# Kernel tuning notes

Measured on AMD Instinct MI355X. Metric: run time of the kernel, lower is better.

Reference implementation:

```python
import jax, jax.numpy as jnp
import numpy as np

HIDDEN = 1024
FFN = 3584
N_EXPERTS = 8
TOP_K = 2


def setup_inputs() -> dict:
    key = jax.random.key(0)
    ks = jax.random.split(key, 5)
    B, S = 2, 2048
    hidden_states = jax.random.normal(ks[0], (B, S, HIDDEN), dtype=jnp.float32)
    # gate: Linear(hidden, n_experts, bias=False); stored as [H, E] so y = x @ gate_w
    gate_w = jax.random.normal(ks[1], (HIDDEN, N_EXPERTS), dtype=jnp.float32) * (HIDDEN ** -0.5)
    # stacked expert weights: w1 (gate proj), w3 (up proj): [E, H, F]; w2 (down proj): [E, F, H]
    w1 = jax.random.normal(ks[2], (N_EXPERTS, HIDDEN, FFN), dtype=jnp.float32) * (HIDDEN ** -0.5)
    w3 = jax.random.normal(ks[3], (N_EXPERTS, HIDDEN, FFN), dtype=jnp.float32) * (HIDDEN ** -0.5)
    w2 = jax.random.normal(ks[4], (N_EXPERTS, FFN, HIDDEN), dtype=jnp.float32) * (FFN ** -0.5)
    return {"hidden_states": hidden_states, "gate_w": gate_w, "w1": w1, "w2": w2, "w3": w3}


def reference(hidden_states, gate_w, w1, w2, w3):
    B, S, H = hidden_states.shape
    x = hidden_states.reshape(-1, H)  # [T, H]
    T = x.shape[0]
    router_logits = x @ gate_w  # [T, E]
    # softmax in fp32 as in original
    routing_weights = jax.nn.softmax(router_logits.astype(jnp.float32), axis=-1)
    top_w, selected = jax.lax.top_k(routing_weights, TOP_K)  # [T, k]
    top_w = top_w / jnp.sum(top_w, axis=-1, keepdims=True)
    top_w = top_w.astype(x.dtype)
    # scatter top-k weights into dense per-expert combine weights [T, E];
    # zero weight for unselected experts reproduces the sparse gather/scatter math exactly
    combine = jnp.zeros((T, N_EXPERTS), dtype=x.dtype).at[
        jnp.arange(T)[:, None], selected
    ].add(top_w)
    # expert gated MLP, all experts batched: [T, E, F]
    g = jnp.einsum('th,ehf->tef', x, w1)
    u = jnp.einsum('th,ehf->tef', x, w3)
    h = jax.nn.silu(g) * u
    # down-proj fused with weighted combine: avoids [T, E, H] intermediate
    final_hidden_states = jnp.einsum('tef,efh,te->th', h, w2, combine)
    return final_hidden_states, router_logits
```

## Files before the change

kernel.cpp:

```cpp
#include <hip/hip_runtime.h>
#include <hip/hip_bf16.h>
#include <cstdint>
#include <cstddef>

#define T_TOK 4096
#define HID   1024
#define FFN   3584
#define FFI   (2 * FFN)
#define NEXP  8
#define RTOT  (T_TOK * 2)
#define MAXT  72
#define BM 128
#define BN 128
#define BK 64
#define NT1 (FFI / BN)
#define NT2 (HID / BN)
#define SPLITK2 2
#define KCH2 (FFN / SPLITK2)
#define CPAD 32

typedef __attribute__((ext_vector_type(8))) short bvec8;
typedef __attribute__((ext_vector_type(4))) short bvec4;
typedef __attribute__((ext_vector_type(4))) float fvec4;
typedef unsigned short u16;

__device__ __forceinline__ u16 f2b(float f) {
  __bf16 b = (__bf16)f;
  return __builtin_bit_cast(u16, b);
}
__device__ __forceinline__ float b2f(u16 u) {
  unsigned v = (unsigned)u << 16;
  return __builtin_bit_cast(float, v);
}

__device__ __forceinline__ void gload16(const u16* g, u16* l) {
  __builtin_amdgcn_global_load_lds((const __attribute__((address_space(1))) void*)g,
                                   (__attribute__((address_space(3))) void*)l, 16, 0, 0);
}

__device__ __forceinline__ int xcd_swz(int bid, int nwg) {
  int q = nwg >> 3, r = nwg & 7;
  int xcd = bid & 7, sub = bid >> 3;
  return (xcd < r ? xcd * (q + 1) : r * (q + 1) + (xcd - r) * q) + sub;
}

__global__ void router_kernel(const float* __restrict__ x, const float* __restrict__ gw,
                              float* __restrict__ logits, int* __restrict__ tk_id,
                              float* __restrict__ tk_w, int* __restrict__ counts,
                              u16* __restrict__ xb, int full) {
  const int lane = threadIdx.x & 63;
  const int wid  = threadIdx.x >> 6;
  const int t = blockIdx.x * 4 + wid;
  const float4* xr = (const float4*)(x + (size_t)t * HID);
  float acc[NEXP] = {0.f, 0.f, 0.f, 0.f, 0.f, 0.f, 0.f, 0.f};
#pragma unroll
  for (int it = 0; it < 4; ++it) {
    int k4 = it * 64 + lane;
    float4 xv = xr[k4];
    if (xb) {
      bvec4 o;
      o[0] = (short)f2b(xv.x); o[1] = (short)f2b(xv.y);
      o[2] = (short)f2b(xv.z); o[3] = (short)f2b(xv.w);
      *(bvec4*)(xb + (size_t)t * HID + k4 * 4) = o;
    }
    const float* gp = gw + (size_t)k4 * 4 * NEXP;
    float xs[4] = {xv.x, xv.y, xv.z, xv.w};
#pragma unroll
    for (int kk = 0; kk < 4; ++kk) {
      float4 ga = ((const float4*)(gp + kk * NEXP))[0];
      float4 gb = ((const float4*)(gp + kk * NEXP))[1];
      acc[0] += xs[kk] * ga.x; acc[1] += xs[kk] * ga.y;
      acc[2] += xs[kk] * ga.z; acc[3] += xs[kk] * ga.w;
      acc[4] += xs[kk] * gb.x; acc[5] += xs[kk] * gb.y;
      acc[6] += xs[kk] * gb.z; acc[7] += xs[kk] * gb.w;
    }
  }
#pragma unroll
  for (int off = 32; off > 0; off >>= 1) {
#pragma unroll
    for (int e = 0; e < NEXP; ++e) acc[e] += __shfl_xor(acc[e], off, 64);
  }
  if (lane < NEXP) logits[(size_t)t * NEXP + lane] = acc[lane];
  if (full && lane == 0) {
    int e0 = 0; float l0 = acc[0];
#pragma unroll
    for (int e = 1; e < NEXP; ++e) if (acc[e] > l0) { l0 = acc[e]; e0 = e; }
    int e1 = -1; float l1 = -3.4e38f;
#pragma unroll
    for (int e = 0; e < NEXP; ++e) if (e != e0 && acc[e] > l1) { l1 = acc[e]; e1 = e; }
    float w0 = 1.f / (1.f + expf(l1 - l0));
    float w1 = 1.f - w0;
    tk_id[t * 2 + 0] = e0; tk_id[t * 2 + 1] = e1;
    tk_w[t * 2 + 0] = w0;  tk_w[t * 2 + 1] = w1;
    atomicAdd(&counts[e0 * CPAD], 1); atomicAdd(&counts[e1 * CPAD], 1);
  }
}

__global__ void scan_kernel(const int* __restrict__ counts, int* __restrict__ offsets,
                            int* __restrict__ cursors, int4* __restrict__ tilemap) {
  __shared__ int c[NEXP];
  __shared__ int tbase[NEXP + 1];
  const int t = threadIdx.x;
  if (t < NEXP) c[t] = counts[t * CPAD];
  __syncthreads();
  if (t < NEXP) {
    int off = 0, tiles = 0;
    for (int e = 0; e < t; ++e) { off += c[e]; tiles += (c[e] + BM - 1) / BM; }
    offsets[t] = off; cursors[t * CPAD] = 0;
    if (t == NEXP - 1) {
      offsets[NEXP] = off + c[t];
      tbase[NEXP] = tiles + (c[t] + BM - 1) / BM;
    }
    tbase[t] = tiles;
    const int cc = c[t];
    for (int tm = 0; tm * BM < cc; ++tm)
      tilemap[tiles + tm] = make_int4(t, off + tm * BM, min(BM, cc - tm * BM), 0);
  }
  __syncthreads();
  for (int i = tbase[NEXP] + t; i < MAXT; i += 64)
    tilemap[i] = make_int4(-1, 0, 0, 0);
}

__global__ void scatter_kernel(const int* __restrict__ tk_id, const float* __restrict__ tk_w,
                               const int* __restrict__ offsets, int* __restrict__ cursors,
                               int* __restrict__ rowmap, float* __restrict__ roww,
                               int* __restrict__ tokrow) {
  int i = blockIdx.x * 256 + threadIdx.x;
  int t = i >> 1;
  int e = tk_id[i]; float w = tk_w[i];
  const int lane = threadIdx.x & 63;
  const unsigned long long lt = (lane == 63) ? ~0ull >> 1 : (1ull << lane) - 1ull;
  int base = 0, rank = 0;
#pragma unroll
  for (int ex = 0; ex < NEXP; ++ex) {
    unsigned long long m = __ballot(e == ex);
    if (e == ex) {
      int cnt = __popcll(m);
      int leader = __ffsll((long long)m) - 1;
      int b = 0;
      if (lane == leader) b = atomicAdd(&cursors[ex * CPAD], cnt);
      b = __shfl(b, leader, 64);
      base = b; rank = __popcll(m & lt);
    }
  }
  int r = offsets[e] + base + rank;
  rowmap[r] = t; roww[r] = w;
  tokrow[i] = r;
}

__global__ void transpose_cast_dual_kernel(const float* __restrict__ w1,
                                           const float* __restrict__ w3,
                                           u16* __restrict__ bi) {
  __shared__ __attribute__((aligned(16))) u16 tile[64 * 72];
  const int z = blockIdx.z, e = z >> 1, half = z & 1;
  const float* src = (half ? w3 : w1) + (size_t)e * HID * FFN;
  u16* dst = bi + (size_t)e * FFI * HID;
  const int c0 = blockIdx.x * 64, r0 = blockIdx.y * 64;
  const int t = threadIdx.x;
  const int m = t & 15;
  const int g = t >> 4;
  u16 v[4][4];
#pragma unroll
  for (int i = 0; i < 4; ++i) {
    float4 q = *(const float4*)(src + (size_t)(r0 + 4 * g + i) * FFN + c0 + 4 * m);
    v[i][0] = f2b(q.x); v[i][1] = f2b(q.y); v[i][2] = f2b(q.z); v[i][3] = f2b(q.w);
  }
  const int phys = (g ^ ((m & 3) << 2)) * 4;
#pragma unroll
  for (int j = 0; j < 4; ++j) {
    int c = 4 * m + j;
    bvec4 o; o[0] = (short)v[0][j]; o[1] = (short)v[1][j];
    o[2] = (short)v[2][j]; o[3] = (short)v[3][j];
    *(bvec4*)&tile[c * 72 + phys] = o;
  }
  __syncthreads();
  const int cl = t >> 2;
  const int q  = t & 3;
  const int base = ((q ^ ((cl >> 2) & 3)) << 4);
  bvec8 ra = *(const bvec8*)&tile[cl * 72 + base];
  bvec8 rb = *(const bvec8*)&tile[cl * 72 + base + 8];
  const int orow = (c0 << 1) + ((cl >> 4) << 5) + (cl & 15) + (half << 4);
  u16* dp = dst + (size_t)orow * HID + r0 + 16 * q;
  *(bvec8*)(dp + 0) = ra;
  *(bvec8*)(dp + 8) = rb;
}

__global__ void transpose_cast_w2_kernel(const float* __restrict__ w2, u16* __restrict__ w2t) {
  __shared__ __attribute__((aligned(16))) u16 tile[64 * 72];
  const int e = blockIdx.z;
  const float* src = w2 + (size_t)e * FFN * HID;
  u16* dst = w2t + (size_t)e * HID * FFN;
  const int c0 = blockIdx.x * 64, r0 = blockIdx.y * 64;
  const int t = threadIdx.x;
  const int m = t & 15;
  const int g = t >> 4;
  u16 v[4][4];
#pragma unroll
  for (int i = 0; i < 4; ++i) {
    float4 q = *(const float4*)(src + (size_t)(r0 + 4 * g + i) * HID + c0 + 4 * m);
    v[i][0] = f2b(q.x); v[i][1] = f2b(q.y); v[i][2] = f2b(q.z); v[i][3] = f2b(q.w);
  }
  const int phys = (g ^ ((m & 3) << 2)) * 4;
#pragma unroll
  for (int j = 0; j < 4; ++j) {
    int c = 4 * m + j;
    bvec4 o; o[0] = (short)v[0][j]; o[1] = (short)v[1][j];
    o[2] = (short)v[2][j]; o[3] = (short)v[3][j];
    *(bvec4*)&tile[c * 72 + phys] = o;
  }
  __syncthreads();
  const int cl = t >> 2;
  const int q  = t & 3;
  const int base = ((q ^ ((cl >> 2) & 3)) << 4);
  bvec8 ra = *(const bvec8*)&tile[cl * 72 + base];
  bvec8 rb = *(const bvec8*)&tile[cl * 72 + base + 8];
  u16* dp = dst + (size_t)(c0 + cl) * FFN + r0 + 16 * q;
  *(bvec8*)(dp + 0) = ra;
  *(bvec8*)(dp + 8) = rb;
}

__launch_bounds__(256, 3)
__global__ void gemm1_kernel(const u16* __restrict__ xb, const u16* __restrict__ bi,
                             const int* __restrict__ rowmap,
                             const int4* __restrict__ tilemap, u16* __restrict__ hbuf) {
  const int wg = xcd_swz(blockIdx.x, NT1 * MAXT);
  const int mt = wg % MAXT;
  const int nt = wg / MAXT;
  int4 ti = tilemap[mt];
  if (ti.x < 0) return;
  const int e = ti.x, rowbase = ti.y, mvalid = ti.z;
  const int n0 = nt * BN;

  __shared__ __attribute__((aligned(128))) u16 As[BM * BK];
  __shared__ __attribute__((aligned(128))) u16 Bs[BN * BK];

  const int tid = threadIdx.x;
  const int lane = tid & 63;
  const int wv = tid >> 6;

  const int srow = tid >> 3;
  const int csrc = ((tid & 7) ^ (srow & 7)) * 8;
  const u16* wb = bi + (size_t)e * FFI * HID;
  const u16* gA[4]; const u16* gB[4];
  u16* lA[4]; u16* lB[4];
#pragma unroll
  for (int r = 0; r < 4; ++r) {
    int row = r * 32 + srow;
    int tok = rowmap[min(rowbase + row, RTOT - 1)];
    gA[r] = xb + (size_t)tok * HID + csrc;
    gB[r] = wb + (size_t)(n0 + row) * HID + csrc;
    lA[r] = &As[(r * 32 + wv * 8) * BK];
    lB[r] = &Bs[(r * 32 + wv * 8) * BK];
  }

  const int wm = (tid >> 7) & 1, wn = (tid >> 6) & 1;
  const int l15 = lane & 15;
  const int kg = lane >> 4;
  const int swz = l15 & 7;
  const int aBase = (wm * 64 + l15) * BK;
  const int bBase = (wn * 64 + l15) * BK;
  const int ch0 = ((0 + kg) ^ swz) * 8;
  const int ch1 = ((4 + kg) ^ swz) * 8;

  fvec4 acc[4][4] = {};

  for (int kt = 0; kt < HID / BK; ++kt) {
#pragma unroll
    for (int r = 0; r < 4; ++r) { gload16(gA[r], lA[r]); gA[r] += BK; }
#pragma unroll
    for (int r = 0; r < 4; ++r) { gload16(gB[r], lB[r]); gB[r] += BK; }
    __syncthreads();
    bvec8 a0[4], a1[4];
#pragma unroll
    for (int mi = 0; mi < 4; ++mi) {
      a0[mi] = *(const bvec8*)&As[aBase + mi * 16 * BK + ch0];
      a1[mi] = *(const bvec8*)&As[aBase + mi * 16 * BK + ch1];
    }
#pragma unroll
    for (int ni = 0; ni < 4; ++ni) {
      bvec8 b0 = *(const bvec8*)&Bs[bBase + ni * 16 * BK + ch0];
#pragma unroll
      for (int mi = 0; mi < 4; ++mi)
        acc[mi][ni] = __builtin_amdgcn_mfma_f32_16x16x32_bf16(a0[mi], b0, acc[mi][ni], 0, 0, 0);
      bvec8 b1 = *(const bvec8*)&Bs[bBase + ni * 16 * BK + ch1];
#pragma unroll
      for (int mi = 0; mi < 4; ++mi)
        acc[mi][ni] = __builtin_amdgcn_mfma_f32_16x16x32_bf16(a1[mi], b1, acc[mi][ni], 0, 0, 0);
    }
    __syncthreads();
  }
  const int rg4 = (lane >> 4) * 4;
#pragma unroll
  for (int mi = 0; mi < 4; ++mi) {
#pragma unroll
    for (int j = 0; j < 4; ++j) {
      int ml = wm * 64 + mi * 16 + rg4 + j;
      if (ml < mvalid) {
        size_t rowoff = (size_t)(rowbase + ml) * FFN + ((n0 + wn * 64) >> 1);
#pragma unroll
        for (int np = 0; np < 2; ++np) {
          float g = acc[mi][2 * np][j], u = acc[mi][2 * np + 1][j];
          float hv = (g / (1.f + expf(-g))) * u;
          hbuf[rowoff + np * 16 + l15] = f2b(hv);
        }
      }
    }
  }
}

__launch_bounds__(256, 3)
__global__ void gemm2_kernel(const u16* __restrict__ hbuf, const u16* __restrict__ w2t,
                             const float* __restrict__ roww,
                             const int4* __restrict__ tilemap, u16* __restrict__ part) {
  const int wg = xcd_swz(blockIdx.x, NT2 * MAXT * SPLITK2);
  const int mt = wg % MAXT;
  const int rest = wg / MAXT;
  const int nt = rest % NT2;
  const int sk = rest / NT2;
  int4 ti = tilemap[mt];
  if (ti.x < 0) return;
  const int e = ti.x, rowbase = ti.y, mvalid = ti.z;
  const int n0 = nt * BN;
  const int k0 = sk * KCH2;

  __shared__ __attribute__((aligned(128))) u16 As[BM * BK];
  __shared__ __attribute__((aligned(128))) u16 Bs[BN * BK];

  const int tid = threadIdx.x;
  const int lane = tid & 63;
  const int wv = tid >> 6;

  const int srow = tid >> 3;
  const int csrc = ((tid & 7) ^ (srow & 7)) * 8;
  const u16* wb2 = w2t + (size_t)e * HID * FFN;
  const u16* gA[4]; const u16* gB[4];
  u16* lA[4]; u16* lB[4];
#pragma unroll
  for (int r = 0; r < 4; ++r) {
    int row = r * 32 + srow;
    gA[r] = hbuf + (size_t)min(rowbase + row, RTOT - 1) * FFN + k0 + csrc;
    gB[r] = wb2 + (size_t)(n0 + row) * FFN + k0 + csrc;
    lA[r] = &As[(r * 32 + wv * 8) * BK];
    lB[r] = &Bs[(r * 32 + wv * 8) * BK];
  }

  const int wm = (tid >> 7) & 1, wn = (tid >> 6) & 1;
  const int l15 = lane & 15;
  const int kg = lane >> 4;
  const int swz = l15 & 7;
  const int aBase = (wm * 64 + l15) * BK;
  const int bBase = (wn * 64 + l15) * BK;
  const int ch0 = ((0 + kg) ^ swz) * 8;
  const int ch1 = ((4 + kg) ^ swz) * 8;

  fvec4 acc[4][4] = {};

  for (int kt = 0; kt < KCH2 / BK; ++kt) {
#pragma unroll
    for (int r = 0; r < 4; ++r) { gload16(gA[r], lA[r]); gA[r] += BK; }
#pragma unroll
    for (int r = 0; r < 4; ++r) { gload16(gB[r], lB[r]); gB[r] += BK; }
    __syncthreads();
    bvec8 a0[4], a1[4];
#pragma unroll
    for (int mi = 0; mi < 4; ++mi) {
      a0[mi] = *(const bvec8*)&As[aBase + mi * 16 * BK + ch0];
      a1[mi] = *(const bvec8*)&As[aBase + mi * 16 * BK + ch1];
    }
#pragma unroll
    for (int ni = 0; ni < 4; ++ni) {
      bvec8 b0 = *(const bvec8*)&Bs[bBase + ni * 16 * BK + ch0];
#pragma unroll
      for (int mi = 0; mi < 4; ++mi)
        acc[mi][ni] = __builtin_amdgcn_mfma_f32_16x16x32_bf16(a0[mi], b0, acc[mi][ni], 0, 0, 0);
      bvec8 b1 = *(const bvec8*)&Bs[bBase + ni * 16 * BK + ch1];
#pragma unroll
      for (int mi = 0; mi < 4; ++mi)
        acc[mi][ni] = __builtin_amdgcn_mfma_f32_16x16x32_bf16(a1[mi], b1, acc[mi][ni], 0, 0, 0);
    }
    __syncthreads();
  }
  u16* pp = part + (size_t)sk * RTOT * HID;
  const int rg4 = (lane >> 4) * 4;
#pragma unroll
  for (int mi = 0; mi < 4; ++mi) {
#pragma unroll
    for (int j = 0; j < 4; ++j) {
      int ml = wm * 64 + mi * 16 + rg4 + j;
      if (ml < mvalid) {
        int r = rowbase + ml;
        float wgt = roww[r];
        u16* op = pp + (size_t)r * HID + n0 + wn * 64;
#pragma unroll
        for (int ni = 0; ni < 4; ++ni)
          op[ni * 16 + l15] = f2b(acc[mi][ni][j] * wgt);
      }
    }
  }
}

__global__ void combine_kernel(const u16* __restrict__ part, const int* __restrict__ tokrow,
                               float* __restrict__ out) {
  int idx = blockIdx.x * 256 + threadIdx.x;
  int t = idx >> 7;
  int c = (idx & 127) * 8;
  int r0 = tokrow[2 * t], r1 = tokrow[2 * t + 1];
  const size_t sk1 = (size_t)RTOT * HID;
  bvec8 a = *(const bvec8*)(part + (size_t)r0 * HID + c);
  bvec8 b = *(const bvec8*)(part + sk1 + (size_t)r0 * HID + c);
  bvec8 d = *(const bvec8*)(part + (size_t)r1 * HID + c);
  bvec8 f = *(const bvec8*)(part + sk1 + (size_t)r1 * HID + c);
  float* dst = out + (size_t)t * HID + c;
#pragma unroll
  for (int k = 0; k < 8; ++k)
    dst[k] = (b2f((u16)a[k]) + b2f((u16)b[k])) + (b2f((u16)d[k]) + b2f((u16)f[k]));
}

extern "C" void kernel_launch(void* const* d_in, const int* in_sizes, int n_in,
                              void* d_out, int out_size, void* d_ws, size_t ws_size,
                              hipStream_t stream) {
  (void)in_sizes; (void)n_in; (void)out_size;
  const float* x  = (const float*)d_in[0];
  const float* gw = (const float*)d_in[1];
  const float* w1 = (const float*)d_in[2];
  const float* w2 = (const float*)d_in[3];
  const float* w3 = (const float*)d_in[4];
  float* out = (float*)d_out;
  float* logits = out + (size_t)T_TOK * HID;

  size_t off = 0;
  auto take = [&](size_t b) { size_t o = off; off += (b + 255) & ~(size_t)255; return o; };
  size_t o_xb   = take((size_t)T_TOK * HID * 2);
  size_t o_wt   = take((size_t)NEXP * FFI * HID * 2);
  size_t o_hb   = take((size_t)RTOT * FFN * 2);
  size_t o_rmap = take((size_t)RTOT * 4);
  size_t o_rw   = take((size_t)RTOT * 4);
  size_t o_tid  = take((size_t)RTOT * 4);
  size_t o_tw   = take((size_t)RTOT * 4);
  size_t o_trow = take((size_t)RTOT * 4);
  size_t o_cnt  = take(4 * NEXP * CPAD);
  size_t o_ofs  = take(4 * (NEXP + 1));
  size_t o_cur  = take(4 * NEXP * CPAD);
  size_t o_tmap = take(MAXT * 16);
  size_t total = off;

  if (ws_size < total) {
    hipMemsetAsync(d_out, 0, (size_t)T_TOK * HID * sizeof(float), stream);
    router_kernel<<<T_TOK / 4, 256, 0, stream>>>(x, gw, logits, nullptr, nullptr, nullptr,
                                                 nullptr, 0);
    return;
  }

  char* w = (char*)d_ws;
  u16* xb   = (u16*)(w + o_xb);
  u16* bi   = (u16*)(w + o_wt);
  u16* w2t  = bi;
  u16* part = bi + (size_t)NEXP * HID * FFN;
  u16* hb   = (u16*)(w + o_hb);
  int*   rmap = (int*)(w + o_rmap);
  float* rw   = (float*)(w + o_rw);
  int*   tkid = (int*)(w + o_tid);
  float* tkw  = (float*)(w + o_tw);
  int*   trow = (int*)(w + o_trow);
  int*   cnt  = (int*)(w + o_cnt);
  int*   ofs  = (int*)(w + o_ofs);
  int*   cur  = (int*)(w + o_cur);
  int4*  tmap = (int4*)(w + o_tmap);

  hipMemsetAsync(cnt, 0, 4 * NEXP * CPAD, stream);
  router_kernel<<<T_TOK / 4, 256, 0, stream>>>(x, gw, logits, tkid, tkw, cnt, xb, 1);
  scan_kernel<<<1, 64, 0, stream>>>(cnt, ofs, cur, tmap);
  scatter_kernel<<<RTOT / 256, 256, 0, stream>>>(tkid, tkw, ofs, cur, rmap, rw, trow);
  transpose_cast_dual_kernel<<<dim3(FFN / 64, HID / 64, 2 * NEXP), 256, 0, stream>>>(w1, w3, bi);
  gemm1_kernel<<<NT1 * MAXT, 256, 0, stream>>>(xb, bi, rmap, tmap, hb);
  transpose_cast_w2_kernel<<<dim3(HID / 64, FFN / 64, NEXP), 256, 0, stream>>>(w2, w2t);
  gemm2_kernel<<<NT2 * MAXT * SPLITK2, 256, 0, stream>>>(hb, w2t, rw, tmap, part);
  combine_kernel<<<T_TOK * HID / 8 / 256, 256, 0, stream>>>(part, trow, out);
}
```

Measured before the change: 384.8 us.

## Merge router with w1/w3 transpose and gemm1 with w2 transpose into fused launches

Combines the router and the w1/w3 transpose-cast into one grid that branches on block index, and likewise runs the w2 transpose-cast blocks alongside the gemm1 blocks in one launch. To make this legal, w2t gets its own workspace region instead of aliasing the w1/w3 buffer that gemm1 reads. The aim is to remove launch gaps and let memory-bound transpose work overlap with router and GEMM compute. The cost is extra workspace and shared fused kernels with a larger grid. The fused kernel uses the gemm1 launch bounds and shared-memory footprint for the transpose blocks.

```diff
diff --git a/kernel.cpp b/kernel.cpp
--- a/kernel.cpp
+++ b/kernel.cpp
@@ -18,6 +18,10 @@
 #define SPLITK2 2
 #define KCH2 (FFN / SPLITK2)
 #define CPAD 32
+#define G1BLKS (NT1 * MAXT)
+#define W2TBLKS ((HID/64)*(FFN/64)*NEXP)
+#define RTRBLKS (T_TOK / 4)
+#define DTBLKS  ((FFN/64)*(HID/64)*2*NEXP)
 
 typedef __attribute__((ext_vector_type(8))) short bvec8;
 typedef __attribute__((ext_vector_type(4))) short bvec4;
@@ -44,13 +48,14 @@
   return (xcd < r ? xcd * (q + 1) : r * (q + 1) + (xcd - r) * q) + sub;
 }
 
-__global__ void router_kernel(const float* __restrict__ x, const float* __restrict__ gw,
-                              float* __restrict__ logits, int* __restrict__ tk_id,
-                              float* __restrict__ tk_w, int* __restrict__ counts,
-                              u16* __restrict__ xb, int full) {
-  const int lane = threadIdx.x & 63;
-  const int wid  = threadIdx.x >> 6;
-  const int t = blockIdx.x * 4 + wid;
+
+__device__ void router_body(const float* __restrict__ x, const float* __restrict__ gw,
+                            float* __restrict__ logits, int* __restrict__ tk_id,
+                            float* __restrict__ tk_w, int* __restrict__ counts,
+                            u16* __restrict__ xb, int blk, int tid) {
+  const int lane = tid & 63;
+  const int wid  = tid >> 6;
+  const int t = blk * 4 + wid;
   const float4* xr = (const float4*)(x + (size_t)t * HID);
   float acc[NEXP] = {0.f, 0.f, 0.f, 0.f, 0.f, 0.f, 0.f, 0.f};
 #pragma unroll
@@ -81,7 +86,7 @@
     for (int e = 0; e < NEXP; ++e) acc[e] += __shfl_xor(acc[e], off, 64);
   }
   if (lane < NEXP) logits[(size_t)t * NEXP + lane] = acc[lane];
-  if (full && lane == 0) {
+  if (tk_id && lane == 0) {
     int e0 = 0; float l0 = acc[0];
 #pragma unroll
     for (int e = 1; e < NEXP; ++e) if (acc[e] > l0) { l0 = acc[e]; e0 = e; }
@@ -94,6 +99,218 @@
     tk_w[t * 2 + 0] = w0;  tk_w[t * 2 + 1] = w1;
     atomicAdd(&counts[e0 * CPAD], 1); atomicAdd(&counts[e1 * CPAD], 1);
   }
+}
+
+__device__ void dualT_body(const float* __restrict__ w1, const float* __restrict__ w3,
+                           u16* __restrict__ bi, int bx, int by, int bz, int t,
+                           u16* __restrict__ tile) {
+  const int e = bz >> 1, half = bz & 1;
+  const float* src = (half ? w3 : w1) + (size_t)e * HID * FFN;
+  u16* dst = bi + (size_t)e * FFI * HID;
+  const int c0 = bx * 64, r0 = by * 64;
+  const int m = t & 15;
+  const int g = t >> 4;
+  u16 v[4][4];
+#pragma unroll
+  for (int i = 0; i < 4; ++i) {
+    float4 q = *(const float4*)(src + (size_t)(r0 + 4 * g + i) * FFN + c0 + 4 * m);
+    v[i][0] = f2b(q.x); v[i][1] = f2b(q.y); v[i][2] = f2b(q.z); v[i][3] = f2b(q.w);
+  }
+  const int phys = (g ^ ((m & 3) << 2)) * 4;
+#pragma unroll
+  for (int j = 0; j < 4; ++j) {
+    int c = 4 * m + j;
+    bvec4 o; o[0] = (short)v[0][j]; o[1] = (short)v[1][j];
+    o[2] = (short)v[2][j]; o[3] = (short)v[3][j];
+    *(bvec4*)&tile[c * 72 + phys] = o;
+  }
+  __syncthreads();
+  const int cl = t >> 2;
+  const int q  = t & 3;
+  const int base = ((q ^ ((cl >> 2) & 3)) << 4);
+  bvec8 ra = *(const bvec8*)&tile[cl * 72 + base];
+  bvec8 rb = *(const bvec8*)&tile[cl * 72 + base + 8];
+  const int orow = (c0 << 1) + ((cl >> 4) << 5) + (cl & 15) + (half << 4);
+  u16* dp = dst + (size_t)orow * HID + r0 + 16 * q;
+  *(bvec8*)(dp + 0) = ra;
+  *(bvec8*)(dp + 8) = rb;
+}
+
+__device__ void w2T_body(const float* __restrict__ w2, u16* __restrict__ w2t,
+                         int bx, int by, int e, int t, u16* __restrict__ tile) {
+  const float* src = w2 + (size_t)e * FFN * HID;
+  u16* dst = w2t + (size_t)e * HID * FFN;
+  const int c0 = bx * 64, r0 = by * 64;
+  const int m = t & 15;
+  const int g = t >> 4;
+  u16 v[4][4];
+#pragma unroll
+  for (int i = 0; i < 4; ++i) {
+    float4 q = *(const float4*)(src + (size_t)(r0 + 4 * g + i) * HID + c0 + 4 * m);
+    v[i][0] = f2b(q.x); v[i][1] = f2b(q.y); v[i][2] = f2b(q.z); v[i][3] = f2b(q.w);
+  }
+  const int phys = (g ^ ((m & 3) << 2)) * 4;
+#pragma unroll
+  for (int j = 0; j < 4; ++j) {
+    int c = 4 * m + j;
+    bvec4 o; o[0] = (short)v[0][j]; o[1] = (short)v[1][j];
+    o[2] = (short)v[2][j]; o[3] = (short)v[3][j];
+    *(bvec4*)&tile[c * 72 + phys] = o;
+  }
+  __syncthreads();
+  const int cl = t >> 2;
+  const int q  = t & 3;
+  const int base = ((q ^ ((cl >> 2) & 3)) << 4);
+  bvec8 ra = *(const bvec8*)&tile[cl * 72 + base];
+  bvec8 rb = *(const bvec8*)&tile[cl * 72 + base + 8];
+  u16* dp = dst + (size_t)(c0 + cl) * FFN + r0 + 16 * q;
+  *(bvec8*)(dp + 0) = ra;
+  *(bvec8*)(dp + 8) = rb;
+}
+
+__device__ void gemm1_body(const u16* __restrict__ xb, const u16* __restrict__ bi,
+                           const int* __restrict__ rowmap, const int4* __restrict__ tilemap,
+                           u16* __restrict__ hbuf, int bid, int tid,
+                           u16* __restrict__ As, u16* __restrict__ Bs) {
+  const int wg = xcd_swz(bid, NT1 * MAXT);
+  const int mt = wg % MAXT;
+  const int nt = wg / MAXT;
+  int4 ti = tilemap[mt];
+  if (ti.x < 0) return;
+  const int e = ti.x, rowbase = ti.y, mvalid = ti.z;
+  const int n0 = nt * BN;
+
+  const int lane = tid & 63;
+  const int wv = tid >> 6;
+  const int srow = tid >> 3;
+  const int csrc = ((tid & 7) ^ (srow & 7)) * 8;
+  const u16* wb = bi + (size_t)e * FFI * HID;
+  const u16* gA[4]; const u16* gB[4];
+  u16* lA[4]; u16* lB[4];
+#pragma unroll
+  for (int r = 0; r < 4; ++r) {
+    int row = r * 32 + srow;
+    int tok = rowmap[min(rowbase + row, RTOT - 1)];
+    gA[r] = xb + (size_t)tok * HID + csrc;
+    gB[r] = wb + (size_t)(n0 + row) * HID + csrc;
+    lA[r] = &As[(r * 32 + wv * 8) * BK];
+    lB[r] = &Bs[(r * 32 + wv * 8) * BK];
+  }
+
+  const int wm = (tid >> 7) & 1, wn = (tid >> 6) & 1;
+  const int l15 = lane & 15;
+  const int kg = lane >> 4;
+  const int swz = l15 & 7;
+  const int aBase = (wm * 64 + l15) * BK;
+  const int bBase = (wn * 64 + l15) * BK;
+  const int ch0 = ((0 + kg) ^ swz) * 8;
+  const int ch1 = ((4 + kg) ^ swz) * 8;
+
+  fvec4 acc[4][4] = {};
+
+  for (int kt = 0; kt < HID / BK; ++kt) {
+#pragma unroll
+    for (int r = 0; r < 4; ++r) { gload16(gA[r], lA[r]); gA[r] += BK; }
+#pragma unroll
+    for (int r = 0; r < 4; ++r) { gload16(gB[r], lB[r]); gB[r] += BK; }
+    __syncthreads();
+    bvec8 a0[4], a1[4];
+#pragma unroll
+    for (int mi = 0; mi < 4; ++mi) {
+      a0[mi] = *(const bvec8*)&As[aBase + mi * 16 * BK + ch0];
+      a1[mi] = *(const bvec8*)&As[aBase + mi * 16 * BK + ch1];
+    }
+#pragma unroll
+    for (int ni = 0; ni < 4; ++ni) {
+      bvec8 b0 = *(const bvec8*)&Bs[bBase + ni * 16 * BK + ch0];
+#pragma unroll
+      for (int mi = 0; mi < 4; ++mi)
+        acc[mi][ni] = __builtin_amdgcn_mfma_f32_16x16x32_bf16(a0[mi], b0, acc[mi][ni], 0, 0, 0);
+      bvec8 b1 = *(const bvec8*)&Bs[bBase + ni * 16 * BK + ch1];
+#pragma unroll
+      for (int mi = 0; mi < 4; ++mi)
+        acc[mi][ni] = __builtin_amdgcn_mfma_f32_16x16x32_bf16(a1[mi], b1, acc[mi][ni], 0, 0, 0);
+    }
+    __syncthreads();
+  }
+  const int rg4 = (lane >> 4) * 4;
+#pragma unroll
+  for (int mi = 0; mi < 4; ++mi) {
+#pragma unroll
+    for (int j = 0; j < 4; ++j) {
+      int ml = wm * 64 + mi * 16 + rg4 + j;
+      if (ml < mvalid) {
+        size_t rowoff = (size_t)(rowbase + ml) * FFN + ((n0 + wn * 64) >> 1);
+#pragma unroll
+        for (int np = 0; np < 2; ++np) {
+          float g = acc[mi][2 * np][j], u = acc[mi][2 * np + 1][j];
+          float hv = (g / (1.f + expf(-g))) * u;
+          hbuf[rowoff + np * 16 + l15] = f2b(hv);
+        }
+      }
+    }
+  }
+}
+
+
+__global__ void fused_pre_kernel(const float* __restrict__ x, const float* __restrict__ gw,
+                                 const float* __restrict__ w1, const float* __restrict__ w3,
+                                 float* __restrict__ logits, int* __restrict__ tk_id,
+                                 float* __restrict__ tk_w, int* __restrict__ counts,
+                                 u16* __restrict__ xb, u16* __restrict__ bi) {
+  __shared__ __attribute__((aligned(16))) u16 tile[64 * 72];
+  const int bid = blockIdx.x;
+  if (bid < RTRBLKS) {
+    router_body(x, gw, logits, tk_id, tk_w, counts, xb, bid, threadIdx.x);
+  } else {
+    int did = bid - RTRBLKS;
+    int bx = did % (FFN / 64); int rest = did / (FFN / 64);
+    int by = rest % (HID / 64); int bz = rest / (HID / 64);
+    dualT_body(w1, w3, bi, bx, by, bz, threadIdx.x, tile);
+  }
+}
+
+__launch_bounds__(256, 3)
+__global__ void fused_g1w2_kernel(const u16* __restrict__ xb, const u16* __restrict__ bi,
+                                  const int* __restrict__ rowmap,
+                                  const int4* __restrict__ tilemap, u16* __restrict__ hbuf,
+                                  const float* __restrict__ w2, u16* __restrict__ w2t) {
+  __shared__ __attribute__((aligned(128))) u16 As[BM * BK];
+  __shared__ __attribute__((aligned(128))) u16 Bs[BN * BK];
+  const int bid = blockIdx.x;
+  if (bid < G1BLKS) {
+    gemm1_body(xb, bi, rowmap, tilemap, hbuf, bid, threadIdx.x, As, Bs);
+  } else {
+    int id = bid - G1BLKS;
+    int bx = id % (HID / 64); int rest = id / (HID / 64);
+    int by = rest % (FFN / 64); int e = rest / (FFN / 64);
+    w2T_body(w2, w2t, bx, by, e, threadIdx.x, As);
+  }
+}
+
+__global__ void router_kernel(const float* __restrict__ x, const float* __restrict__ gw,
+                              float* __restrict__ logits, int* __restrict__ tk_id,
+                              float* __restrict__ tk_w, int* __restrict__ counts,
+                              u16* __restrict__ xb) {
+  router_body(x, gw, logits, tk_id, tk_w, counts, xb, blockIdx.x, threadIdx.x);
+}
+__global__ void transpose_cast_dual_kernel(const float* __restrict__ w1,
+                                           const float* __restrict__ w3,
+                                           u16* __restrict__ bi) {
+  __shared__ __attribute__((aligned(16))) u16 tile[64 * 72];
+  dualT_body(w1, w3, bi, blockIdx.x, blockIdx.y, blockIdx.z, threadIdx.x, tile);
+}
+__global__ void transpose_cast_w2_kernel(const float* __restrict__ w2, u16* __restrict__ w2t) {
+  __shared__ __attribute__((aligned(16))) u16 tile[64 * 72];
+  w2T_body(w2, w2t, blockIdx.x, blockIdx.y, blockIdx.z, threadIdx.x, tile);
+}
+__launch_bounds__(256, 3)
+__global__ void gemm1_kernel(const u16* __restrict__ xb, const u16* __restrict__ bi,
+                             const int* __restrict__ rowmap,
+                             const int4* __restrict__ tilemap, u16* __restrict__ hbuf) {
+  __shared__ __attribute__((aligned(128))) u16 As[BM * BK];
+  __shared__ __attribute__((aligned(128))) u16 Bs[BN * BK];
+  gemm1_body(xb, bi, rowmap, tilemap, hbuf, blockIdx.x, threadIdx.x, As, Bs);
 }
 
 __global__ void scan_kernel(const int* __restrict__ counts, int* __restrict__ offsets,
@@ -148,166 +365,6 @@
   tokrow[i] = r;
 }
 
-__global__ void transpose_cast_dual_kernel(const float* __restrict__ w1,
-                                           const float* __restrict__ w3,
-                                           u16* __restrict__ bi) {
-  __shared__ __attribute__((aligned(16))) u16 tile[64 * 72];
-  const int z = blockIdx.z, e = z >> 1, half = z & 1;
-  const float* src = (half ? w3 : w1) + (size_t)e * HID * FFN;
-  u16* dst = bi + (size_t)e * FFI * HID;
-  const int c0 = blockIdx.x * 64, r0 = blockIdx.y * 64;
-  const int t = threadIdx.x;
-  const int m = t & 15;
-  const int g = t >> 4;
-  u16 v[4][4];
-#pragma unroll
-  for (int i = 0; i < 4; ++i) {
-    float4 q = *(const float4*)(src + (size_t)(r0 + 4 * g + i) * FFN + c0 + 4 * m);
-    v[i][0] = f2b(q.x); v[i][1] = f2b(q.y); v[i][2] = f2b(q.z); v[i][3] = f2b(q.w);
-  }
-  const int phys = (g ^ ((m & 3) << 2)) * 4;
-#pragma unroll
-  for (int j = 0; j < 4; ++j) {
-    int c = 4 * m + j;
-    bvec4 o; o[0] = (short)v[0][j]; o[1] = (short)v[1][j];
-    o[2] = (short)v[2][j]; o[3] = (short)v[3][j];
-    *(bvec4*)&tile[c * 72 + phys] = o;
-  }
-  __syncthreads();
-  const int cl = t >> 2;
-  const int q  = t & 3;
-  const int base = ((q ^ ((cl >> 2) & 3)) << 4);
-  bvec8 ra = *(const bvec8*)&tile[cl * 72 + base];
-  bvec8 rb = *(const bvec8*)&tile[cl * 72 + base + 8];
-  const int orow = (c0 << 1) + ((cl >> 4) << 5) + (cl & 15) + (half << 4);
-  u16* dp = dst + (size_t)orow * HID + r0 + 16 * q;
-  *(bvec8*)(dp + 0) = ra;
-  *(bvec8*)(dp + 8) = rb;
-}
-
-__global__ void transpose_cast_w2_kernel(const float* __restrict__ w2, u16* __restrict__ w2t) {
-  __shared__ __attribute__((aligned(16))) u16 tile[64 * 72];
-  const int e = blockIdx.z;
-  const float* src = w2 + (size_t)e * FFN * HID;
-  u16* dst = w2t + (size_t)e * HID * FFN;
-  const int c0 = blockIdx.x * 64, r0 = blockIdx.y * 64;
-  const int t = threadIdx.x;
-  const int m = t & 15;
-  const int g = t >> 4;
-  u16 v[4][4];
-#pragma unroll
-  for (int i = 0; i < 4; ++i) {
-    float4 q = *(const float4*)(src + (size_t)(r0 + 4 * g + i) * HID + c0 + 4 * m);
-    v[i][0] = f2b(q.x); v[i][1] = f2b(q.y); v[i][2] = f2b(q.z); v[i][3] = f2b(q.w);
-  }
-  const int phys = (g ^ ((m & 3) << 2)) * 4;
-#pragma unroll
-  for (int j = 0; j < 4; ++j) {
-    int c = 4 * m + j;
-    bvec4 o; o[0] = (short)v[0][j]; o[1] = (short)v[1][j];
-    o[2] = (short)v[2][j]; o[3] = (short)v[3][j];
-    *(bvec4*)&tile[c * 72 + phys] = o;
-  }
-  __syncthreads();
-  const int cl = t >> 2;
-  const int q  = t & 3;
-  const int base = ((q ^ ((cl >> 2) & 3)) << 4);
-  bvec8 ra = *(const bvec8*)&tile[cl * 72 + base];
-  bvec8 rb = *(const bvec8*)&tile[cl * 72 + base + 8];
-  u16* dp = dst + (size_t)(c0 + cl) * FFN + r0 + 16 * q;
-  *(bvec8*)(dp + 0) = ra;
-  *(bvec8*)(dp + 8) = rb;
-}
-
-__launch_bounds__(256, 3)
-__global__ void gemm1_kernel(const u16* __restrict__ xb, const u16* __restrict__ bi,
-                             const int* __restrict__ rowmap,
-                             const int4* __restrict__ tilemap, u16* __restrict__ hbuf) {
-  const int wg = xcd_swz(blockIdx.x, NT1 * MAXT);
-  const int mt = wg % MAXT;
-  const int nt = wg / MAXT;
-  int4 ti = tilemap[mt];
-  if (ti.x < 0) return;
-  const int e = ti.x, rowbase = ti.y, mvalid = ti.z;
-  const int n0 = nt * BN;
-
-  __shared__ __attribute__((aligned(128))) u16 As[BM * BK];
-  __shared__ __attribute__((aligned(128))) u16 Bs[BN * BK];
-
-  const int tid = threadIdx.x;
-  const int lane = tid & 63;
-  const int wv = tid >> 6;
-
-  const int srow = tid >> 3;
-  const int csrc = ((tid & 7) ^ (srow & 7)) * 8;
-  const u16* wb = bi + (size_t)e * FFI * HID;
-  const u16* gA[4]; const u16* gB[4];
-  u16* lA[4]; u16* lB[4];
-#pragma unroll
-  for (int r = 0; r < 4; ++r) {
-    int row = r * 32 + srow;
-    int tok = rowmap[min(rowbase + row, RTOT - 1)];
-    gA[r] = xb + (size_t)tok * HID + csrc;
-    gB[r] = wb + (size_t)(n0 + row) * HID + csrc;
-    lA[r] = &As[(r * 32 + wv * 8) * BK];
-    lB[r] = &Bs[(r * 32 + wv * 8) * BK];
-  }
-
-  const int wm = (tid >> 7) & 1, wn = (tid >> 6) & 1;
-  const int l15 = lane & 15;
-  const int kg = lane >> 4;
-  const int swz = l15 & 7;
-  const int aBase = (wm * 64 + l15) * BK;
-  const int bBase = (wn * 64 + l15) * BK;
-  const int ch0 = ((0 + kg) ^ swz) * 8;
-  const int ch1 = ((4 + kg) ^ swz) * 8;
-
-  fvec4 acc[4][4] = {};
-
-  for (int kt = 0; kt < HID / BK; ++kt) {
-#pragma unroll
-    for (int r = 0; r < 4; ++r) { gload16(gA[r], lA[r]); gA[r] += BK; }
-#pragma unroll
-    for (int r = 0; r < 4; ++r) { gload16(gB[r], lB[r]); gB[r] += BK; }
-    __syncthreads();
-    bvec8 a0[4], a1[4];
-#pragma unroll
-    for (int mi = 0; mi < 4; ++mi) {
-      a0[mi] = *(const bvec8*)&As[aBase + mi * 16 * BK + ch0];
-      a1[mi] = *(const bvec8*)&As[aBase + mi * 16 * BK + ch1];
-    }
-#pragma unroll
-    for (int ni = 0; ni < 4; ++ni) {
-      bvec8 b0 = *(const bvec8*)&Bs[bBase + ni * 16 * BK + ch0];
-#pragma unroll
-      for (int mi = 0; mi < 4; ++mi)
-        acc[mi][ni] = __builtin_amdgcn_mfma_f32_16x16x32_bf16(a0[mi], b0, acc[mi][ni], 0, 0, 0);
-      bvec8 b1 = *(const bvec8*)&Bs[bBase + ni * 16 * BK + ch1];
-#pragma unroll
-      for (int mi = 0; mi < 4; ++mi)
-        acc[mi][ni] = __builtin_amdgcn_mfma_f32_16x16x32_bf16(a1[mi], b1, acc[mi][ni], 0, 0, 0);
-    }
-    __syncthreads();
-  }
-  const int rg4 = (lane >> 4) * 4;
-#pragma unroll
-  for (int mi = 0; mi < 4; ++mi) {
-#pragma unroll
-    for (int j = 0; j < 4; ++j) {
-      int ml = wm * 64 + mi * 16 + rg4 + j;
-      if (ml < mvalid) {
-        size_t rowoff = (size_t)(rowbase + ml) * FFN + ((n0 + wn * 64) >> 1);
-#pragma unroll
-        for (int np = 0; np < 2; ++np) {
-          float g = acc[mi][2 * np][j], u = acc[mi][2 * np + 1][j];
-          float hv = (g / (1.f + expf(-g))) * u;
-          hbuf[rowoff + np * 16 + l15] = f2b(hv);
-        }
-      }
-    }
-  }
-}
-
 __launch_bounds__(256, 3)
 __global__ void gemm2_kernel(const u16* __restrict__ hbuf, const u16* __restrict__ w2t,
                              const float* __restrict__ roww,
@@ -442,19 +499,21 @@
   size_t o_ofs  = take(4 * (NEXP + 1));
   size_t o_cur  = take(4 * NEXP * CPAD);
   size_t o_tmap = take(MAXT * 16);
-  size_t total = off;
-
-  if (ws_size < total) {
+  size_t total_base = off;
+  size_t o_w2t  = take((size_t)NEXP * HID * FFN * 2);
+  size_t total_fused = off;
+
+  if (ws_size < total_base) {
     hipMemsetAsync(d_out, 0, (size_t)T_TOK * HID * sizeof(float), stream);
-    router_kernel<<<T_TOK / 4, 256, 0, stream>>>(x, gw, logits, nullptr, nullptr, nullptr,
-                                                 nullptr, 0);
+    router_kernel<<<RTRBLKS, 256, 0, stream>>>(x, gw, logits, nullptr, nullptr, nullptr,
+                                               nullptr);
     return;
   }
+  const bool fused = (ws_size >= total_fused);
 
   char* w = (char*)d_ws;
   u16* xb   = (u16*)(w + o_xb);
   u16* bi   = (u16*)(w + o_wt);
-  u16* w2t  = bi;
   u16* part = bi + (size_t)NEXP * HID * FFN;
   u16* hb   = (u16*)(w + o_hb);
   int*   rmap = (int*)(w + o_rmap);
@@ -466,14 +525,23 @@
   int*   ofs  = (int*)(w + o_ofs);
   int*   cur  = (int*)(w + o_cur);
   int4*  tmap = (int4*)(w + o_tmap);
+  u16* w2t = fused ? (u16*)(w + o_w2t) : bi;
 
   hipMemsetAsync(cnt, 0, 4 * NEXP * CPAD, stream);
-  router_kernel<<<T_TOK / 4, 256, 0, stream>>>(x, gw, logits, tkid, tkw, cnt, xb, 1);
-  scan_kernel<<<1, 64, 0, stream>>>(cnt, ofs, cur, tmap);
-  scatter_kernel<<<RTOT / 256, 256, 0, stream>>>(tkid, tkw, ofs, cur, rmap, rw, trow);
-  transpose_cast_dual_kernel<<<dim3(FFN / 64, HID / 64, 2 * NEXP), 256, 0, stream>>>(w1, w3, bi);
-  gemm1_kernel<<<NT1 * MAXT, 256, 0, stream>>>(xb, bi, rmap, tmap, hb);
-  transpose_cast_w2_kernel<<<dim3(HID / 64, FFN / 64, NEXP), 256, 0, stream>>>(w2, w2t);
+  if (fused) {
+    fused_pre_kernel<<<RTRBLKS + DTBLKS, 256, 0, stream>>>(x, gw, w1, w3, logits, tkid, tkw,
+                                                           cnt, xb, bi);
+    scan_kernel<<<1, 64, 0, stream>>>(cnt, ofs, cur, tmap);
+    scatter_kernel<<<RTOT / 256, 256, 0, stream>>>(tkid, tkw, ofs, cur, rmap, rw, trow);
+    fused_g1w2_kernel<<<G1BLKS + W2TBLKS, 256, 0, stream>>>(xb, bi, rmap, tmap, hb, w2, w2t);
+  } else {
+    router_kernel<<<RTRBLKS, 256, 0, stream>>>(x, gw, logits, tkid, tkw, cnt, xb);
+    scan_kernel<<<1, 64, 0, stream>>>(cnt, ofs, cur, tmap);
+    scatter_kernel<<<RTOT / 256, 256, 0, stream>>>(tkid, tkw, ofs, cur, rmap, rw, trow);
+    transpose_cast_dual_kernel<<<dim3(FFN / 64, HID / 64, 2 * NEXP), 256, 0, stream>>>(w1, w3, bi);
+    gemm1_kernel<<<G1BLKS, 256, 0, stream>>>(xb, bi, rmap, tmap, hb);
+    transpose_cast_w2_kernel<<<dim3(HID / 64, FFN / 64, NEXP), 256, 0, stream>>>(w2, w2t);
+  }
   gemm2_kernel<<<NT2 * MAXT * SPLITK2, 256, 0, stream>>>(hb, w2t, rw, tmap, part);
   combine_kernel<<<T_TOK * HID / 8 / 256, 256, 0, stream>>>(part, trow, out);
 }
```

Result: no change. 385.0 us (median of 2 runs) (+0.0%).
